# Performance work log

Measured on AMD Instinct MI355X. Metric: run time of the kernel, lower is better.

Reference implementation:

```python
import jax, jax.numpy as jnp
import numpy as np

# Constants matching module reset(): R_reset=5 -> R = 5+15 = 20; T = 10.0; kn=0, gn=1
G = 128          # grid_side
N = G * G        # 16384 cells
R = 20
NB = (2 * R + 3) ** 2        # 1849 = nb_neighbors per the module's assert
NSHIFT = (2 * R + 1) ** 2    # 1681 slots actually filled by the shift loop
T = 10.0
NB_RULES = 4


def _neighbor_idx():
    idx = np.arange(N)
    i, j = idx // G, idx % G
    si, sj = np.meshgrid(np.arange(-R, R + 1), np.arange(-R, R + 1), indexing='ij')
    si, sj = si.ravel(), sj.ravel()   # row-major: shift_i outer loop, shift_j inner
    nb = ((i[:, None] + si[None, :]) % G) * G + (j[:, None] + sj[None, :]) % G  # [N, NSHIFT]
    full = np.zeros((N, NB), dtype=np.int32)   # unfilled slots default to cell 0 (as in torch zeros init)
    full[:, :NSHIFT] = nb
    return jnp.asarray(full)

NEI = _neighbor_idx()   # [N, NB] int32, translation-invariant periodic neighbor list


def setup_inputs() -> dict:
    key = jax.random.key(0)
    ks = jax.random.split(key, 9)
    idx = jnp.arange(N)
    pos = jnp.stack([idx // G, idx % G], axis=-1).astype(jnp.float32)   # [N, 2] grid coords
    x = jax.random.uniform(ks[0], (N, 3), dtype=jnp.float32)            # [N, C] state in [0,1]
    c0 = jax.random.randint(ks[1], (NB_RULES,), 0, 3)                   # source channel per rule
    c1 = jax.random.randint(ks[2], (NB_RULES,), 0, 3)                   # target channel per rule
    r = 0.5 + 0.5 * jax.random.uniform(ks[3], (NB_RULES,), dtype=jnp.float32)
    rk = jax.random.uniform(ks[4], (NB_RULES, 3), dtype=jnp.float32)    # kernel ring centers
    b = jax.random.uniform(ks[5], (NB_RULES, 3), dtype=jnp.float32)     # kernel ring heights
    w = 0.1 + 0.4 * jax.random.uniform(ks[6], (NB_RULES, 3), dtype=jnp.float32)  # ring widths
    h = jax.random.uniform(ks[7], (NB_RULES,), dtype=jnp.float32)       # growth strength
    m = 0.1 + 0.4 * jax.random.uniform(ks[8], (NB_RULES,), dtype=jnp.float32)    # growth mean
    s = 0.05 + 0.1 * jax.random.uniform(jax.random.fold_in(key, 99), (NB_RULES,), dtype=jnp.float32)
    return {"pos": pos, "x": x, "c0": c0, "c1": c1, "r": r, "rk": rk,
            "b": b, "w": w, "h": h, "m": m, "s": s}


def reference(pos, x, c0, c1, r, rk, b, w, h, m, s):
    # gather neighbor states: x_ext[:, 0] is self, rest are the NB neighbors -> [N, 1+NB, C]
    x_ext = jnp.concatenate([x[:, None, :], x[NEI]], axis=1)
    # translation-invariant distance computed at the center cell (as in torch)
    center = G * G // 2 + G // 2
    dpos = jnp.concatenate([jnp.zeros((1, 2), pos.dtype), pos[NEI[center]] - pos[center]], axis=0)  # [1+NB, 2]
    dist = jnp.sqrt(jnp.sum(dpos ** 2, axis=-1)) / R   # [1+NB]
    edge_mask = jax.nn.sigmoid(-(dist - 1.0) * 10.0)
    delta_x = jnp.zeros_like(x)
    for k in range(NB_RULES):
        # kernel_core[0]: sum of Gaussian rings over the last axis
        wk = edge_mask * (b[k] * jnp.exp(-((dist[:, None] / r[k] - rk[k]) / w[k]) ** 2 / 2)).sum(-1)  # [1+NB]
        wn = wk / wk.sum()                    # per-cell weight rows are identical -> compute once
        potential = jnp.mean(wn[None, :] * x_ext[:, :, c0[k]], axis=1)   # aggr='mean' -> [N]
        # field_func[1]
        field = jnp.exp(-(potential - m[k]) ** 2 / (2 * s[k] ** 2) - 0.001) * 2 - 1
        delta_x = delta_x.at[:, c1[k]].add(h[k] * field)
    new_x = jnp.clip(x + delta_x / T, 0.0, 1.0)
    return pos, new_x
```

## Files before the change

kernel.cpp:

```cpp
#include <hip/hip_runtime.h>
#include <math.h>

#define G 128
#define NCELLS (G*G)
#define RAD 20
#define NS 41
#define NTAPS (NS*NS)
#define NB_FULL 1850.0f
#define NTAIL 168.0f
#define NRULES 4
#define NQ 4
#define QROWPAD 44
#define QROWS 11
#define QSZ (QROWS*QROWPAD)
#define CONV_BLOCKS 256

#define WOFF_TAIL 0
#define WOFF_POT  16
#define WOFF_BW   (WOFF_POT + NRULES*NQ*NCELLS)

__device__ __forceinline__ float kw(float d, float irk,
                                    float rk0, float rk1, float rk2,
                                    float b0, float b1, float b2,
                                    float iw0, float iw1, float iw2) {
    float em = 1.f / (1.f + __expf((d - 1.f) * 10.f));
    float dd = d * irk;
    float u0 = (dd - rk0) * iw0;
    float u1 = (dd - rk1) * iw1;
    float u2 = (dd - rk2) * iw2;
    return em * (b0 * __expf(-0.5f * u0 * u0)
               + b1 * __expf(-0.5f * u1 * u1)
               + b2 * __expf(-0.5f * u2 * u2));
}

__global__ __launch_bounds__(256)
void lenia_conv(const float* __restrict__ x,
                const int* __restrict__ c0v,
                const float* __restrict__ rr,
                const float* __restrict__ rkv,
                const float* __restrict__ bv,
                const float* __restrict__ wv,
                float* __restrict__ ws) {
    __shared__ __align__(16) float xt[18*168];
    __shared__ float red[4];

    const int bid  = blockIdx.x;
    const int q    = bid & 3;
    const int k    = (bid >> 2) & 3;
    const int tile = bid >> 4;
    const int i0   = tile * 8;
    const int t    = threadIdx.x;
    const int si0  = (q == 0) ? 0 : (q * 10 + 1);
    const int nsi  = (q == 0) ? 11 : 10;
    const int r0   = i0 - RAD + si0;
    const int NR   = nsi + 7;
    const int ck   = c0v[k];

    for (int idx = t; idx < NR * 168; idx += 256) {
        int rrow = idx / 168;
        int cc   = idx - rrow * 168;
        int grow = (r0 + rrow) & (G - 1);
        int gcol = (cc - 20) & (G - 1);
        xt[rrow*168 + cc] = x[grow*(G*3) + gcol*3 + ck];
    }

    const float irk = 1.f / rr[k];
    const float rk0 = rkv[k*3+0], rk1 = rkv[k*3+1], rk2 = rkv[k*3+2];
    const float b0  = bv[k*3+0],  b1  = bv[k*3+1],  b2  = bv[k*3+2];
    const float iw0 = 1.f / wv[k*3+0], iw1 = 1.f / wv[k*3+1], iw2 = 1.f / wv[k*3+2];
    const float invR = 1.f / (float)RAD;

    float vals[7];
    float lsum = 0.f;
    #pragma unroll
    for (int j = 0; j < 7; ++j) {
        int sidx = t + j * 256;
        float wk = 0.f;
        if (sidx < NTAPS) {
            int si = sidx / NS - RAD;
            int sj = sidx % NS - RAD;
            float d = sqrtf((float)(si*si + sj*sj)) * invR;
            wk = kw(d, irk, rk0, rk1, rk2, b0, b1, b2, iw0, iw1, iw2);
        }
        vals[j] = wk;
        lsum += wk;
    }
    #pragma unroll
    for (int mm = 32; mm > 0; mm >>= 1) lsum += __shfl_xor(lsum, mm, 64);
    if ((t & 63) == 0) red[t >> 6] = lsum;
    __syncthreads();
    const float S4 = red[0] + red[1] + red[2] + red[3];
    const float wself = kw(0.f, irk, rk0, rk1, rk2, b0, b1, b2, iw0, iw1, iw2);
    const float dtail = sqrtf(8192.f) * invR;
    const float wtail = kw(dtail, irk, rk0, rk1, rk2, b0, b1, b2, iw0, iw1, iw2);
    const float S = S4 + wself + NTAIL * wtail;
    const float inv = 1.f / (S * NB_FULL);

    float* bw = ws + WOFF_BW + bid * QSZ;
    const int lo = si0 * NS, hi = (si0 + nsi) * NS;
    #pragma unroll
    for (int j = 0; j < 7; ++j) {
        int sidx = t + j * 256;
        if (sidx >= lo && sidx < hi) {
            float v = vals[j] * inv;
            if (sidx == RAD*NS + RAD) v += wself * inv;
            int l = sidx - lo;
            bw[(l / NS) * QROWPAD + (l % NS)] = v;
        }
    }
    if (t < QROWS * 3) bw[(t / 3) * QROWPAD + NS + (t % 3)] = 0.f;
    if (tile == 0 && q == 0 && t == 0) ws[WOFF_TAIL + k] = NTAIL * wtail * inv;
    __syncthreads();

    const int row = t >> 5;
    const int cb  = (t & 31) * 4;
    float a0 = 0.f, a1 = 0.f, a2 = 0.f, a3 = 0.f;

    for (int ii = 0; ii < nsi; ++ii) {
        const float* rp = &xt[(row + ii)*168 + cb];
        float wwin[44];
        #pragma unroll
        for (int u = 0; u < 11; ++u) {
            float4 v = *(const float4*)&rp[4*u];
            wwin[4*u] = v.x; wwin[4*u+1] = v.y; wwin[4*u+2] = v.z; wwin[4*u+3] = v.w;
        }
        const float* wr = bw + ii * QROWPAD;
        float wrow[44];
        #pragma unroll
        for (int u = 0; u < 11; ++u) {
            float4 v = *(const float4*)&wr[4*u];
            wrow[4*u] = v.x; wrow[4*u+1] = v.y; wrow[4*u+2] = v.z; wrow[4*u+3] = v.w;
        }
        #pragma unroll
        for (int s2 = 0; s2 < 41; ++s2) {
            a0 = fmaf(wrow[s2], wwin[s2],   a0);
            a1 = fmaf(wrow[s2], wwin[s2+1], a1);
            a2 = fmaf(wrow[s2], wwin[s2+2], a2);
            a3 = fmaf(wrow[s2], wwin[s2+3], a3);
        }
    }

    int cell = (i0 + row) * G + cb;
    float4 res; res.x = a0; res.y = a1; res.z = a2; res.w = a3;
    *(float4*)&ws[WOFF_POT + (k * NQ + q) * NCELLS + cell] = res;
}

__global__ __launch_bounds__(256)
void lenia_update(const float* __restrict__ pos,
                  const float* __restrict__ x,
                  const int* __restrict__ c0v,
                  const int* __restrict__ c1v,
                  const float* __restrict__ hv,
                  const float* __restrict__ mv,
                  const float* __restrict__ sv,
                  const float* __restrict__ ws,
                  float* __restrict__ out) {
    int n = blockIdx.x * 256 + threadIdx.x;
    *(float2*)&out[2*n] = *(const float2*)&pos[2*n];

    float xv0 = x[n*3 + 0], xv1 = x[n*3 + 1], xv2 = x[n*3 + 2];
    float d0 = 0.f, d1 = 0.f, d2 = 0.f;
    #pragma unroll
    for (int kk = 0; kk < NRULES; ++kk) {
        float pot = ws[WOFF_TAIL + kk] * x[c0v[kk]];
        #pragma unroll
        for (int qq = 0; qq < NQ; ++qq)
            pot += ws[WOFF_POT + (kk * NQ + qq) * NCELLS + n];
        float u = pot - mv[kk];
        float sk = sv[kk];
        float field = __expf(-u*u / (2.f * sk * sk) - 0.001f) * 2.f - 1.f;
        float add = hv[kk] * field;
        int c = c1v[kk];
        if (c == 0) d0 += add; else if (c == 1) d1 += add; else d2 += add;
    }
    float* ox = out + 2 * NCELLS;
    ox[n*3 + 0] = fminf(fmaxf(xv0 + d0 * 0.1f, 0.f), 1.f);
    ox[n*3 + 1] = fminf(fmaxf(xv1 + d1 * 0.1f, 0.f), 1.f);
    ox[n*3 + 2] = fminf(fmaxf(xv2 + d2 * 0.1f, 0.f), 1.f);
}

extern "C" void kernel_launch(void* const* d_in, const int* in_sizes, int n_in,
                              void* d_out, int out_size, void* d_ws, size_t ws_size,
                              hipStream_t stream) {
    const float* pos = (const float*)d_in[0];
    const float* x   = (const float*)d_in[1];
    const int*   c0  = (const int*)  d_in[2];
    const int*   c1  = (const int*)  d_in[3];
    const float* r   = (const float*)d_in[4];
    const float* rk  = (const float*)d_in[5];
    const float* b   = (const float*)d_in[6];
    const float* w   = (const float*)d_in[7];
    const float* h   = (const float*)d_in[8];
    const float* m   = (const float*)d_in[9];
    const float* s   = (const float*)d_in[10];
    float* out = (float*)d_out;
    float* ws  = (float*)d_ws;

    lenia_conv<<<CONV_BLOCKS, 256, 0, stream>>>(x, c0, r, rk, b, w, ws);
    lenia_update<<<NCELLS/256, 256, 0, stream>>>(pos, x, c0, c1, h, m, s, ws, out);
}
```

Measured before the change: 22.75 us.

## Fuse convolution and update into one kernel with in-block row-split reduction

Replaces the two-kernel pipeline (conv writing 16 partial potential planes, then an update pass) with a single kernel. Each of 512 blocks handles 32 cells of one row, loads all three channels for a 41x72 halo into shared memory, computes all four rule kernels, splits the 41 tap rows across 32 thread groups, and reduces partials in shared memory before applying the growth update. This removes a launch and the global round-trip of partial potentials. In exchange, each block recomputes all kernel weights (27 exps per lane per rule), reduction is serialized over 32 threads, and only 32 threads do the final update.

```diff
diff --git a/kernel.cpp b/kernel.cpp
--- a/kernel.cpp
+++ b/kernel.cpp
@@ -9,15 +9,14 @@
 #define NB_FULL 1850.0f
 #define NTAIL 168.0f
 #define NRULES 4
-#define NQ 4
-#define QROWPAD 44
-#define QROWS 11
-#define QSZ (QROWS*QROWPAD)
-#define CONV_BLOCKS 256
-
-#define WOFF_TAIL 0
-#define WOFF_POT  16
-#define WOFF_BW   (WOFF_POT + NRULES*NQ*NCELLS)
+
+#define CELLS_PB 32
+#define COLS 72
+#define PLANE (NS*COLS)
+#define SROWPAD 44
+#define BWSZ (NRULES*NS*SROWPAD)
+#define NGRP 32
+#define NBLOCKS 512
 
 __device__ __forceinline__ float kw(float d, float irk,
                                     float rk0, float rk1, float rk2,
@@ -33,150 +32,172 @@
                + b2 * __expf(-0.5f * u2 * u2));
 }
 
+#define CROW(rq, wq, wq1, A)                                                      \
+    A.x = fmaf(rq.x, wq.x,  A.x); A.y = fmaf(rq.x, wq.y,  A.y);                   \
+    A.z = fmaf(rq.x, wq.z,  A.z); A.w = fmaf(rq.x, wq.w,  A.w);                   \
+    A.x = fmaf(rq.y, wq.y,  A.x); A.y = fmaf(rq.y, wq.z,  A.y);                   \
+    A.z = fmaf(rq.y, wq.w,  A.z); A.w = fmaf(rq.y, wq1.x, A.w);                   \
+    A.x = fmaf(rq.z, wq.z,  A.x); A.y = fmaf(rq.z, wq.w,  A.y);                   \
+    A.z = fmaf(rq.z, wq1.x, A.z); A.w = fmaf(rq.z, wq1.y, A.w);                   \
+    A.x = fmaf(rq.w, wq.w,  A.x); A.y = fmaf(rq.w, wq1.x, A.y);                   \
+    A.z = fmaf(rq.w, wq1.y, A.z); A.w = fmaf(rq.w, wq1.z, A.w);
+
 __global__ __launch_bounds__(256)
-void lenia_conv(const float* __restrict__ x,
-                const int* __restrict__ c0v,
-                const float* __restrict__ rr,
-                const float* __restrict__ rkv,
-                const float* __restrict__ bv,
-                const float* __restrict__ wv,
-                float* __restrict__ ws) {
-    __shared__ __align__(16) float xt[18*168];
-    __shared__ float red[4];
-
-    const int bid  = blockIdx.x;
-    const int q    = bid & 3;
-    const int k    = (bid >> 2) & 3;
-    const int tile = bid >> 4;
-    const int i0   = tile * 8;
-    const int t    = threadIdx.x;
-    const int si0  = (q == 0) ? 0 : (q * 10 + 1);
-    const int nsi  = (q == 0) ? 11 : 10;
-    const int r0   = i0 - RAD + si0;
-    const int NR   = nsi + 7;
-    const int ck   = c0v[k];
-
-    for (int idx = t; idx < NR * 168; idx += 256) {
-        int rrow = idx / 168;
-        int cc   = idx - rrow * 168;
-        int grow = (r0 + rrow) & (G - 1);
-        int gcol = (cc - 20) & (G - 1);
-        xt[rrow*168 + cc] = x[grow*(G*3) + gcol*3 + ck];
-    }
-
-    const float irk = 1.f / rr[k];
-    const float rk0 = rkv[k*3+0], rk1 = rkv[k*3+1], rk2 = rkv[k*3+2];
-    const float b0  = bv[k*3+0],  b1  = bv[k*3+1],  b2  = bv[k*3+2];
-    const float iw0 = 1.f / wv[k*3+0], iw1 = 1.f / wv[k*3+1], iw2 = 1.f / wv[k*3+2];
-    const float invR = 1.f / (float)RAD;
-
-    float vals[7];
-    float lsum = 0.f;
+void lenia_fused(const float* __restrict__ pos,
+                 const float* __restrict__ x,
+                 const int* __restrict__ c0v,
+                 const int* __restrict__ c1v,
+                 const float* __restrict__ rr,
+                 const float* __restrict__ rkv,
+                 const float* __restrict__ bv,
+                 const float* __restrict__ wv,
+                 const float* __restrict__ hv,
+                 const float* __restrict__ mv,
+                 const float* __restrict__ sv,
+                 float* __restrict__ ws,
+                 float* __restrict__ out) {
+    __shared__ __align__(16) float xs[3*PLANE];
+    __shared__ float stail[NRULES];
+
+    const int bid = blockIdx.x;
+    const int t   = threadIdx.x;
+    const int i   = bid >> 2;
+    const int c0  = (bid & 3) * CELLS_PB;
+
+    {
+        int base = bid * 64;
+        if (t < 64) out[base + t] = pos[base + t];
+    }
+
+    for (int idx = t; idx < NS * COLS; idx += 256) {
+        int rrow = idx / COLS;
+        int cc   = idx - rrow * COLS;
+        int grow = (i - RAD + rrow) & (G - 1);
+        int gcol = (c0 - RAD + cc) & (G - 1);
+        const float* xp = x + (grow * G + gcol) * 3;
+        float v0 = xp[0], v1 = xp[1], v2 = xp[2];
+        xs[0*PLANE + idx] = v0;
+        xs[1*PLANE + idx] = v1;
+        xs[2*PLANE + idx] = v2;
+    }
+
+    {
+        const int w    = t >> 6;
+        const int lane = t & 63;
+        const float irk = 1.f / rr[w];
+        const float rk0 = rkv[w*3+0], rk1 = rkv[w*3+1], rk2 = rkv[w*3+2];
+        const float b0  = bv[w*3+0],  b1  = bv[w*3+1],  b2  = bv[w*3+2];
+        const float iw0 = 1.f / wv[w*3+0], iw1 = 1.f / wv[w*3+1], iw2 = 1.f / wv[w*3+2];
+        const float invR = 1.f / (float)RAD;
+
+        float vals[27];
+        float lsum = 0.f;
+        #pragma unroll
+        for (int j = 0; j < 27; ++j) {
+            int sidx = j * 64 + lane;
+            float wk = 0.f;
+            if (sidx < NTAPS) {
+                int si = sidx / NS - RAD;
+                int sj = sidx % NS - RAD;
+                float d = sqrtf((float)(si*si + sj*sj)) * invR;
+                wk = kw(d, irk, rk0, rk1, rk2, b0, b1, b2, iw0, iw1, iw2);
+            }
+            vals[j] = wk;
+            lsum += wk;
+        }
+        #pragma unroll
+        for (int mm = 32; mm > 0; mm >>= 1) lsum += __shfl_xor(lsum, mm, 64);
+        const float wself = kw(0.f, irk, rk0, rk1, rk2, b0, b1, b2, iw0, iw1, iw2);
+        const float dtail = sqrtf(8192.f) * invR;
+        const float wtail = kw(dtail, irk, rk0, rk1, rk2, b0, b1, b2, iw0, iw1, iw2);
+        const float S = lsum + wself + NTAIL * wtail;
+        const float inv = 1.f / (S * NB_FULL);
+
+        float* bwr = ws + (size_t)bid * BWSZ + w * NS * SROWPAD;
+        #pragma unroll
+        for (int j = 0; j < 27; ++j) {
+            int sidx = j * 64 + lane;
+            if (sidx < NTAPS) {
+                float v = vals[j] * inv;
+                if (sidx == RAD*NS + RAD) v += wself * inv;
+                bwr[(sidx / NS) * SROWPAD + (sidx % NS)] = v;
+            }
+        }
+        for (int j = lane; j < NS * 3; j += 64)
+            bwr[(j / 3) * SROWPAD + NS + (j % 3)] = 0.f;
+        if (lane == 0) stail[w] = NTAIL * wtail * inv;
+    }
+    __syncthreads();
+
+    const int g   = t >> 3;
+    const int lc  = t & 7;
+    const int nsi = (g < 9) ? 2 : 1;
+    const int si0 = (g < 9) ? 2*g : 18 + (g - 9);
+
+    float4 acc[4];
     #pragma unroll
-    for (int j = 0; j < 7; ++j) {
-        int sidx = t + j * 256;
-        float wk = 0.f;
-        if (sidx < NTAPS) {
-            int si = sidx / NS - RAD;
-            int sj = sidx % NS - RAD;
-            float d = sqrtf((float)(si*si + sj*sj)) * invR;
-            wk = kw(d, irk, rk0, rk1, rk2, b0, b1, b2, iw0, iw1, iw2);
-        }
-        vals[j] = wk;
-        lsum += wk;
-    }
+    for (int k = 0; k < 4; ++k) { acc[k].x = 0.f; acc[k].y = 0.f; acc[k].z = 0.f; acc[k].w = 0.f; }
+
     #pragma unroll
-    for (int mm = 32; mm > 0; mm >>= 1) lsum += __shfl_xor(lsum, mm, 64);
-    if ((t & 63) == 0) red[t >> 6] = lsum;
+    for (int k = 0; k < 4; ++k) {
+        const int ck = c0v[k];
+        const float* plane = xs + ck * PLANE;
+        const float* bk = ws + (size_t)bid * BWSZ + k * NS * SROWPAD;
+        #pragma unroll
+        for (int ii = 0; ii < 2; ++ii) {
+            if (ii < nsi) {
+                const float4* wp = (const float4*)(plane + (si0 + ii) * COLS + lc * 4);
+                const float4* rp = (const float4*)(bk + (si0 + ii) * SROWPAD);
+                float4 w0 = wp[0], w1 = wp[1], w2 = wp[2], w3 = wp[3], w4 = wp[4], w5 = wp[5];
+                float4 w6 = wp[6], w7 = wp[7], w8 = wp[8], w9 = wp[9], w10 = wp[10];
+                float4 r0 = rp[0], r1 = rp[1], r2 = rp[2], r3 = rp[3], r4 = rp[4], r5 = rp[5];
+                float4 r6 = rp[6], r7 = rp[7], r8 = rp[8], r9 = rp[9], r10 = rp[10];
+                CROW(r0, w0, w1, acc[k])  CROW(r1, w1, w2, acc[k])
+                CROW(r2, w2, w3, acc[k])  CROW(r3, w3, w4, acc[k])
+                CROW(r4, w4, w5, acc[k])  CROW(r5, w5, w6, acc[k])
+                CROW(r6, w6, w7, acc[k])  CROW(r7, w7, w8, acc[k])
+                CROW(r8, w8, w9, acc[k])  CROW(r9, w9, w10, acc[k])
+                acc[k].x = fmaf(r10.x, w10.x, acc[k].x);
+                acc[k].y = fmaf(r10.x, w10.y, acc[k].y);
+                acc[k].z = fmaf(r10.x, w10.z, acc[k].z);
+                acc[k].w = fmaf(r10.x, w10.w, acc[k].w);
+            }
+        }
+    }
     __syncthreads();
-    const float S4 = red[0] + red[1] + red[2] + red[3];
-    const float wself = kw(0.f, irk, rk0, rk1, rk2, b0, b1, b2, iw0, iw1, iw2);
-    const float dtail = sqrtf(8192.f) * invR;
-    const float wtail = kw(dtail, irk, rk0, rk1, rk2, b0, b1, b2, iw0, iw1, iw2);
-    const float S = S4 + wself + NTAIL * wtail;
-    const float inv = 1.f / (S * NB_FULL);
-
-    float* bw = ws + WOFF_BW + bid * QSZ;
-    const int lo = si0 * NS, hi = (si0 + nsi) * NS;
+
+    float* P = xs;
     #pragma unroll
-    for (int j = 0; j < 7; ++j) {
-        int sidx = t + j * 256;
-        if (sidx >= lo && sidx < hi) {
-            float v = vals[j] * inv;
-            if (sidx == RAD*NS + RAD) v += wself * inv;
-            int l = sidx - lo;
-            bw[(l / NS) * QROWPAD + (l % NS)] = v;
-        }
-    }
-    if (t < QROWS * 3) bw[(t / 3) * QROWPAD + NS + (t % 3)] = 0.f;
-    if (tile == 0 && q == 0 && t == 0) ws[WOFF_TAIL + k] = NTAIL * wtail * inv;
+    for (int k = 0; k < 4; ++k) {
+        int base = ((k * NGRP + g) << 5) + lc * 4;
+        P[base + 0] = acc[k].x;
+        P[base + 1] = acc[k].y;
+        P[base + 2] = acc[k].z;
+        P[base + 3] = acc[k].w;
+    }
     __syncthreads();
 
-    const int row = t >> 5;
-    const int cb  = (t & 31) * 4;
-    float a0 = 0.f, a1 = 0.f, a2 = 0.f, a3 = 0.f;
-
-    for (int ii = 0; ii < nsi; ++ii) {
-        const float* rp = &xt[(row + ii)*168 + cb];
-        float wwin[44];
-        #pragma unroll
-        for (int u = 0; u < 11; ++u) {
-            float4 v = *(const float4*)&rp[4*u];
-            wwin[4*u] = v.x; wwin[4*u+1] = v.y; wwin[4*u+2] = v.z; wwin[4*u+3] = v.w;
-        }
-        const float* wr = bw + ii * QROWPAD;
-        float wrow[44];
-        #pragma unroll
-        for (int u = 0; u < 11; ++u) {
-            float4 v = *(const float4*)&wr[4*u];
-            wrow[4*u] = v.x; wrow[4*u+1] = v.y; wrow[4*u+2] = v.z; wrow[4*u+3] = v.w;
-        }
-        #pragma unroll
-        for (int s2 = 0; s2 < 41; ++s2) {
-            a0 = fmaf(wrow[s2], wwin[s2],   a0);
-            a1 = fmaf(wrow[s2], wwin[s2+1], a1);
-            a2 = fmaf(wrow[s2], wwin[s2+2], a2);
-            a3 = fmaf(wrow[s2], wwin[s2+3], a3);
-        }
-    }
-
-    int cell = (i0 + row) * G + cb;
-    float4 res; res.x = a0; res.y = a1; res.z = a2; res.w = a3;
-    *(float4*)&ws[WOFF_POT + (k * NQ + q) * NCELLS + cell] = res;
-}
-
-__global__ __launch_bounds__(256)
-void lenia_update(const float* __restrict__ pos,
-                  const float* __restrict__ x,
-                  const int* __restrict__ c0v,
-                  const int* __restrict__ c1v,
-                  const float* __restrict__ hv,
-                  const float* __restrict__ mv,
-                  const float* __restrict__ sv,
-                  const float* __restrict__ ws,
-                  float* __restrict__ out) {
-    int n = blockIdx.x * 256 + threadIdx.x;
-    *(float2*)&out[2*n] = *(const float2*)&pos[2*n];
-
-    float xv0 = x[n*3 + 0], xv1 = x[n*3 + 1], xv2 = x[n*3 + 2];
-    float d0 = 0.f, d1 = 0.f, d2 = 0.f;
-    #pragma unroll
-    for (int kk = 0; kk < NRULES; ++kk) {
-        float pot = ws[WOFF_TAIL + kk] * x[c0v[kk]];
-        #pragma unroll
-        for (int qq = 0; qq < NQ; ++qq)
-            pot += ws[WOFF_POT + (kk * NQ + qq) * NCELLS + n];
-        float u = pot - mv[kk];
-        float sk = sv[kk];
-        float field = __expf(-u*u / (2.f * sk * sk) - 0.001f) * 2.f - 1.f;
-        float add = hv[kk] * field;
-        int c = c1v[kk];
-        if (c == 0) d0 += add; else if (c == 1) d1 += add; else d2 += add;
-    }
-    float* ox = out + 2 * NCELLS;
-    ox[n*3 + 0] = fminf(fmaxf(xv0 + d0 * 0.1f, 0.f), 1.f);
-    ox[n*3 + 1] = fminf(fmaxf(xv1 + d1 * 0.1f, 0.f), 1.f);
-    ox[n*3 + 2] = fminf(fmaxf(xv2 + d2 * 0.1f, 0.f), 1.f);
+    if (t < CELLS_PB) {
+        int cell = i * G + c0 + t;
+        float xv0 = x[cell*3 + 0], xv1 = x[cell*3 + 1], xv2 = x[cell*3 + 2];
+        float d0 = 0.f, d1 = 0.f, d2 = 0.f;
+        #pragma unroll
+        for (int k = 0; k < 4; ++k) {
+            float pot = stail[k] * x[c0v[k]];
+            for (int g2 = 0; g2 < NGRP; ++g2)
+                pot += P[((k * NGRP + g2) << 5) + t];
+            float u = pot - mv[k];
+            float sk = sv[k];
+            float field = __expf(-u*u / (2.f * sk * sk) - 0.001f) * 2.f - 1.f;
+            float add = hv[k] * field;
+            int c = c1v[k];
+            if (c == 0) d0 += add; else if (c == 1) d1 += add; else d2 += add;
+        }
+        float* ox = out + 2 * NCELLS;
+        ox[cell*3 + 0] = fminf(fmaxf(xv0 + d0 * 0.1f, 0.f), 1.f);
+        ox[cell*3 + 1] = fminf(fmaxf(xv1 + d1 * 0.1f, 0.f), 1.f);
+        ox[cell*3 + 2] = fminf(fmaxf(xv2 + d2 * 0.1f, 0.f), 1.f);
+    }
 }
 
 extern "C" void kernel_launch(void* const* d_in, const int* in_sizes, int n_in,
@@ -196,6 +217,5 @@
     float* out = (float*)d_out;
     float* ws  = (float*)d_ws;
 
-    lenia_conv<<<CONV_BLOCKS, 256, 0, stream>>>(x, c0, r, rk, b, w, ws);
-    lenia_update<<<NCELLS/256, 256, 0, stream>>>(pos, x, c0, c1, h, m, s, ws, out);
+    lenia_fused<<<NBLOCKS, 256, 0, stream>>>(pos, x, c0, c1, r, rk, b, w, h, m, s, ws, out);
 }
```

New measurement: 25.80 us. +13.4%, slower.
